# Kernel tuning notes

Hardware: AMD Instinct MI355X
Metric: run time of the kernel (lower is better)

The kernel has to match this reference:

```python
import jax, jax.numpy as jnp
import numpy as np

B, N, IN_C, HID_C, OUT_C = 64, 1024, 16, 64, 32


def process_graph(graph):
    # graph: [B, N, N]; add self-loops, then row-normalize by inverse degree.
    n = graph.shape[-1]
    g = graph + jnp.eye(n, dtype=graph.dtype)
    deg = jnp.sum(g, axis=-1)                      # [B, N]
    inv_deg = jnp.where(deg == 0, jnp.zeros_like(deg), 1.0 / deg)
    # diag(inv_deg) @ g == row-wise broadcast scale (avoids O(N^3) diag matmul)
    return g * inv_deg[..., None]                  # [B, N, N]


def setup_inputs() -> dict:
    key = jax.random.key(0)
    kx, kg, k1, kb1, k2, kb2 = jax.random.split(key, 6)
    x = jax.random.normal(kx, (B, N, IN_C), dtype=jnp.float32)
    graph = jax.random.uniform(kg, (B, N, N), dtype=jnp.float32)
    # nn.Linear default init: U(-1/sqrt(fan_in), 1/sqrt(fan_in))
    lim1 = 1.0 / np.sqrt(IN_C)
    W1 = jax.random.uniform(k1, (HID_C, IN_C), minval=-lim1, maxval=lim1, dtype=jnp.float32)
    b1 = jax.random.uniform(kb1, (HID_C,), minval=-lim1, maxval=lim1, dtype=jnp.float32)
    lim2 = 1.0 / np.sqrt(HID_C)
    W2 = jax.random.uniform(k2, (OUT_C, HID_C), minval=-lim2, maxval=lim2, dtype=jnp.float32)
    b2 = jax.random.uniform(kb2, (OUT_C,), minval=-lim2, maxval=lim2, dtype=jnp.float32)
    return {"x": x, "graph": graph, "W1": W1, "b1": b1, "W2": W2, "b2": b2}


def reference(x, graph, W1, b1, W2, b2):
    g = process_graph(graph)                                   # [B, N, N]
    h = jnp.einsum('bnc,hc->bnh', x, W1) + b1                  # linear_1
    h = jax.nn.relu(jnp.einsum('bnm,bmh->bnh', g, h))          # propagate + ReLU
    o = jnp.einsum('bnh,oh->bno', h, W2) + b2                  # linear_2
    o = jax.nn.relu(jnp.einsum('bnm,bmo->bno', g, o))          # propagate + ReLU
    return o                                                   # [B, N, OUT_C]
```

## Files before the change

### kernel.cpp

```cpp
#include <hip/hip_runtime.h>

typedef __attribute__((ext_vector_type(8))) short s16x8;
typedef __attribute__((ext_vector_type(8))) unsigned short u16x8;
typedef __attribute__((ext_vector_type(4))) float f32x4;

#define B_   64
#define N_   1024
#define CIN_ 16
#define CH_  64
#define CO_  32

__device__ __forceinline__ unsigned short f2bf(float f){
  unsigned int u = __float_as_uint(f);
  u += 0x7fffu + ((u >> 16) & 1u);
  return (unsigned short)(u >> 16);
}

__global__ __launch_bounds__(256) void k_linear1(
    const float* __restrict__ x, const float* __restrict__ W1,
    const float* __restrict__ b1, unsigned short* __restrict__ H1T){
  int gt   = blockIdx.x * 256 + threadIdx.x;
  int wave = gt >> 6;
  int lane = gt & 63;
  int b    = wave >> 4;
  int nl0  = (wave & 15) << 6;

  const float4* xv = (const float4*)(x + ((size_t)(b * N_ + nl0 + lane)) * CIN_);
  float xr[16];
#pragma unroll
  for (int i = 0; i < 4; ++i){
    float4 v = xv[i];
    xr[i*4+0] = v.x; xr[i*4+1] = v.y; xr[i*4+2] = v.z; xr[i*4+3] = v.w;
  }
  for (int h = 0; h < CH_; ++h){
    float acc = b1[h];
#pragma unroll
    for (int c = 0; c < CIN_; ++c) acc += xr[c] * W1[h * CIN_ + c];
    H1T[((size_t)(b * CH_ + h)) * N_ + nl0 + lane] = f2bf(acc);
  }
}

__global__ __launch_bounds__(256) void k_prop1(
    const float* __restrict__ graph, const unsigned short* __restrict__ H1T,
    const float* __restrict__ W2, const float* __restrict__ b2,
    unsigned short* __restrict__ O1T, float* __restrict__ idegw){
  __shared__ unsigned short sA[64 * 64];
  __shared__ unsigned short sB[64 * 64];
  __shared__ unsigned short sH2[64 * 64];
  __shared__ float sDegP[4 * 64];
  __shared__ float sIdeg[64];

  const int b    = blockIdx.x >> 4;
  const int mblk = blockIdx.x & 15;
  const int m0   = mblk << 6;
  const int tid  = threadIdx.x;
  const int lane = tid & 63, w = tid >> 6;
  const int l15  = lane & 15, lk = lane >> 4;
  const int srow = tid >> 2,  kq = tid & 3;
  const int gn   = m0 + srow;
  const int swzS = (srow & 7) << 3;
  const int swzF = (l15  & 7) << 3;

  const float*          gRow = graph + ((size_t)b << 20) + ((size_t)gn << 10) + (kq << 4);
  const unsigned short* hRow = H1T + ((size_t)(b * CH_ + srow)) * N_ + (kq << 4);

  float degp = 0.f;
  f32x4 acc[4] = {{0,0,0,0},{0,0,0,0},{0,0,0,0},{0,0,0,0}};

  float4 pg[4]; u16x8 ph[2];
  {
    const float4* gp = (const float4*)gRow;
#pragma unroll
    for (int i = 0; i < 4; ++i) pg[i] = gp[i];
    const u16x8* hp = (const u16x8*)hRow;
    ph[0] = hp[0]; ph[1] = hp[1];
  }

  for (int ks = 0; ks < 16; ++ks){
    float4 ng[4]; u16x8 nh[2];
    if (ks < 15){
      const float4* gp = (const float4*)(gRow + ((ks + 1) << 6));
#pragma unroll
      for (int i = 0; i < 4; ++i) ng[i] = gp[i];
      const u16x8* hp = (const u16x8*)(hRow + ((ks + 1) << 6));
      nh[0] = hp[0]; nh[1] = hp[1];
    } else {
#pragma unroll
      for (int i = 0; i < 4; ++i) ng[i] = pg[i];
      nh[0] = ph[0]; nh[1] = ph[1];
    }

    float vals[16];
#pragma unroll
    for (int i = 0; i < 4; ++i){
      float4 v = pg[i];
      if (ks == mblk){
        int gc = (ks << 6) + (kq << 4) + (i << 2);
        v.x += (gc + 0 == gn) ? 1.f : 0.f;
        v.y += (gc + 1 == gn) ? 1.f : 0.f;
        v.z += (gc + 2 == gn) ? 1.f : 0.f;
        v.w += (gc + 3 == gn) ? 1.f : 0.f;
      }
      degp += (v.x + v.y) + (v.z + v.w);
      vals[i*4+0] = v.x; vals[i*4+1] = v.y; vals[i*4+2] = v.z; vals[i*4+3] = v.w;
    }
    u16x8 pk0, pk1;
#pragma unroll
    for (int e = 0; e < 8; ++e){ pk0[e] = f2bf(vals[e]); pk1[e] = f2bf(vals[8 + e]); }
    *(u16x8*)&sA[srow * 64 + (((kq << 4) + 0) ^ swzS)] = pk0;
    *(u16x8*)&sA[srow * 64 + (((kq << 4) + 8) ^ swzS)] = pk1;
    *(u16x8*)&sB[srow * 64 + (((kq << 4) + 0) ^ swzS)] = ph[0];
    *(u16x8*)&sB[srow * 64 + (((kq << 4) + 8) ^ swzS)] = ph[1];
    __syncthreads();
#pragma unroll
    for (int kk = 0; kk < 2; ++kk){
      int ko = (kk << 5) + (lk << 3);
      s16x8 a = *(const s16x8*)&sA[((w << 4) + l15) * 64 + (ko ^ swzF)];
#pragma unroll
      for (int cf = 0; cf < 4; ++cf){
        s16x8 bb = *(const s16x8*)&sB[((cf << 4) + l15) * 64 + (ko ^ swzF)];
        acc[cf] = __builtin_amdgcn_mfma_f32_16x16x32_bf16(a, bb, acc[cf], 0, 0, 0);
      }
    }
    __syncthreads();
#pragma unroll
    for (int i = 0; i < 4; ++i) pg[i] = ng[i];
    ph[0] = nh[0]; ph[1] = nh[1];
  }

  sDegP[(kq << 6) + srow] = degp;
  __syncthreads();
  if (tid < 64){
    float d  = sDegP[tid] + sDegP[64 + tid] + sDegP[128 + tid] + sDegP[192 + tid];
    float id = 1.f / d;
    sIdeg[tid] = id;
    idegw[(b << 10) + m0 + tid] = id;
  }
  __syncthreads();

  f32x4 idv = *(const f32x4*)&sIdeg[(w << 4) + (lk << 2)];
#pragma unroll
  for (int cf = 0; cf < 4; ++cf){
#pragma unroll
    for (int j = 0; j < 4; ++j){
      float hv = acc[cf][j] * idv[j];
      hv = hv > 0.f ? hv : 0.f;
      int row = (w << 4) + (lk << 2) + j;
      int col = (cf << 4) + l15;
      sH2[row * 64 + (col ^ ((row & 7) << 3))] = f2bf(hv);
    }
  }
  __syncthreads();

  f32x4 acc2[2] = {{0,0,0,0},{0,0,0,0}};
#pragma unroll
  for (int kk = 0; kk < 2; ++kk){
    int ko = (kk << 5) + (lk << 3);
    s16x8 a2 = *(const s16x8*)&sH2[((w << 4) + l15) * 64 + (ko ^ swzF)];
#pragma unroll
    for (int cf = 0; cf < 2; ++cf){
      const float4* wv = (const float4*)(W2 + ((cf << 4) + l15) * CH_ + ko);
      float4 w0 = wv[0], w1 = wv[1];
      s16x8 bw;
      bw[0] = (short)f2bf(w0.x); bw[1] = (short)f2bf(w0.y);
      bw[2] = (short)f2bf(w0.z); bw[3] = (short)f2bf(w0.w);
      bw[4] = (short)f2bf(w1.x); bw[5] = (short)f2bf(w1.y);
      bw[6] = (short)f2bf(w1.z); bw[7] = (short)f2bf(w1.w);
      acc2[cf] = __builtin_amdgcn_mfma_f32_16x16x32_bf16(a2, bw, acc2[cf], 0, 0, 0);
    }
  }
#pragma unroll
  for (int cf = 0; cf < 2; ++cf){
    float badd = b2[(cf << 4) + l15];
#pragma unroll
    for (int j = 0; j < 4; ++j){
      float v = acc2[cf][j] + badd;
      int n = m0 + (w << 4) + (lk << 2) + j;
      O1T[((size_t)(b * CO_ + (cf << 4) + l15)) * N_ + n] = f2bf(v);
    }
  }
}

__global__ __launch_bounds__(256) void k_prop2(
    const float* __restrict__ graph, const unsigned short* __restrict__ O1T,
    const float* __restrict__ idegw, float* __restrict__ out){
  __shared__ unsigned short sA[64 * 64];
  __shared__ unsigned short sB[32 * 64];
  __shared__ float sIdeg[64];

  const int b    = blockIdx.x >> 4;
  const int mblk = blockIdx.x & 15;
  const int m0   = mblk << 6;
  const int tid  = threadIdx.x;
  const int lane = tid & 63, w = tid >> 6;
  const int l15  = lane & 15, lk = lane >> 4;
  const int srow = tid >> 2,  kq = tid & 3;
  const int gn   = m0 + srow;
  const int swzS = (srow & 7) << 3;
  const int swzF = (l15  & 7) << 3;

  if (tid < 64) sIdeg[tid] = idegw[(b << 10) + m0 + tid];

  const float* gRow = graph + ((size_t)b << 20) + ((size_t)gn << 10) + (kq << 4);
  const int bcolS = tid >> 3, bkq = tid & 7;
  const unsigned short* oRow = O1T + ((size_t)(b * CO_ + bcolS)) * N_ + (bkq << 3);
  const int swzB = (bcolS & 7) << 3;

  f32x4 acc[2] = {{0,0,0,0},{0,0,0,0}};

  float4 pg[4]; u16x8 po;
  {
    const float4* gp = (const float4*)gRow;
#pragma unroll
    for (int i = 0; i < 4; ++i) pg[i] = gp[i];
    po = *(const u16x8*)oRow;
  }

  for (int ks = 0; ks < 16; ++ks){
    float4 ng[4]; u16x8 no;
    if (ks < 15){
      const float4* gp = (const float4*)(gRow + ((ks + 1) << 6));
#pragma unroll
      for (int i = 0; i < 4; ++i) ng[i] = gp[i];
      no = *(const u16x8*)(oRow + ((ks + 1) << 6));
    } else {
#pragma unroll
      for (int i = 0; i < 4; ++i) ng[i] = pg[i];
      no = po;
    }

    float vals[16];
#pragma unroll
    for (int i = 0; i < 4; ++i){
      float4 v = pg[i];
      if (ks == mblk){
        int gc = (ks << 6) + (kq << 4) + (i << 2);
        v.x += (gc + 0 == gn) ? 1.f : 0.f;
        v.y += (gc + 1 == gn) ? 1.f : 0.f;
        v.z += (gc + 2 == gn) ? 1.f : 0.f;
        v.w += (gc + 3 == gn) ? 1.f : 0.f;
      }
      vals[i*4+0] = v.x; vals[i*4+1] = v.y; vals[i*4+2] = v.z; vals[i*4+3] = v.w;
    }
    u16x8 pk0, pk1;
#pragma unroll
    for (int e = 0; e < 8; ++e){ pk0[e] = f2bf(vals[e]); pk1[e] = f2bf(vals[8 + e]); }
    *(u16x8*)&sA[srow * 64 + (((kq << 4) + 0) ^ swzS)] = pk0;
    *(u16x8*)&sA[srow * 64 + (((kq << 4) + 8) ^ swzS)] = pk1;
    *(u16x8*)&sB[bcolS * 64 + ((bkq << 3) ^ swzB)] = po;
    __syncthreads();
#pragma unroll
    for (int kk = 0; kk < 2; ++kk){
      int ko = (kk << 5) + (lk << 3);
      s16x8 a = *(const s16x8*)&sA[((w << 4) + l15) * 64 + (ko ^ swzF)];
#pragma unroll
      for (int cf = 0; cf < 2; ++cf){
        s16x8 bb = *(const s16x8*)&sB[((cf << 4) + l15) * 64 + (ko ^ swzF)];
        acc[cf] = __builtin_amdgcn_mfma_f32_16x16x32_bf16(a, bb, acc[cf], 0, 0, 0);
      }
    }
    __syncthreads();
#pragma unroll
    for (int i = 0; i < 4; ++i) pg[i] = ng[i];
    po = no;
  }

  f32x4 idv = *(const f32x4*)&sIdeg[(w << 4) + (lk << 2)];
#pragma unroll
  for (int cf = 0; cf < 2; ++cf){
#pragma unroll
    for (int j = 0; j < 4; ++j){
      float v = acc[cf][j] * idv[j];
      v = v > 0.f ? v : 0.f;
      int n = m0 + (w << 4) + (lk << 2) + j;
      out[((size_t)(b * N_ + n)) * CO_ + (cf << 4) + l15] = v;
    }
  }
}

extern "C" void kernel_launch(void* const* d_in, const int* in_sizes, int n_in,
                              void* d_out, int out_size, void* d_ws, size_t ws_size,
                              hipStream_t stream){
  (void)in_sizes; (void)n_in; (void)out_size; (void)ws_size;
  const float* x     = (const float*)d_in[0];
  const float* graph = (const float*)d_in[1];
  const float* W1    = (const float*)d_in[2];
  const float* b1    = (const float*)d_in[3];
  const float* W2    = (const float*)d_in[4];
  const float* b2    = (const float*)d_in[5];
  float* out = (float*)d_out;

  unsigned short* H1T = (unsigned short*)d_ws;
  unsigned short* O1T = (unsigned short*)((char*)d_ws + ((size_t)8 << 20));
  float*        idegw = (float*)((char*)d_ws + ((size_t)12 << 20));

  k_linear1<<<256, 256, 0, stream>>>(x, W1, b1, H1T);
  k_prop1<<<B_ * 16, 256, 0, stream>>>(graph, H1T, W2, b2, O1T, idegw);
  k_prop2<<<B_ * 16, 256, 0, stream>>>(graph, O1T, idegw, out);
}
```

Measured before the change: 451.3 us.

## Load MFMA operands directly from global, dropping LDS staging and barriers

Both propagation kernels now have each lane load its MFMA A fragment (graph row slice) and B fragments (H1T/O1T) straight from global memory in register layout. This removes the LDS tile staging and the two block barriers per k-step. Degree is recomputed in each kernel with wave shuffles instead of being passed through workspace. Graph loads are nontemporal. Each lane's loads are now 32-byte strips per row rather than wide coalesced rows, the B operand is re-read by all four waves, and the loop runs twice as many shorter k-steps.

```diff
diff --git a/kernel.cpp b/kernel.cpp
--- a/kernel.cpp
+++ b/kernel.cpp
@@ -25,12 +25,13 @@
   int b    = wave >> 4;
   int nl0  = (wave & 15) << 6;
 
-  const float4* xv = (const float4*)(x + ((size_t)(b * N_ + nl0 + lane)) * CIN_);
+  const f32x4* xv = (const f32x4*)(x + ((size_t)(b * N_ + nl0 + lane)) * CIN_);
   float xr[16];
 #pragma unroll
   for (int i = 0; i < 4; ++i){
-    float4 v = xv[i];
-    xr[i*4+0] = v.x; xr[i*4+1] = v.y; xr[i*4+2] = v.z; xr[i*4+3] = v.w;
+    f32x4 v = xv[i];
+#pragma unroll
+    for (int e = 0; e < 4; ++e) xr[i*4+e] = v[e];
   }
   for (int h = 0; h < CH_; ++h){
     float acc = b1[h];
@@ -43,130 +44,94 @@
 __global__ __launch_bounds__(256) void k_prop1(
     const float* __restrict__ graph, const unsigned short* __restrict__ H1T,
     const float* __restrict__ W2, const float* __restrict__ b2,
-    unsigned short* __restrict__ O1T, float* __restrict__ idegw){
-  __shared__ unsigned short sA[64 * 64];
-  __shared__ unsigned short sB[64 * 64];
-  __shared__ unsigned short sH2[64 * 64];
-  __shared__ float sDegP[4 * 64];
-  __shared__ float sIdeg[64];
+    unsigned short* __restrict__ O1T){
+  __shared__ unsigned short sH2[4][16 * 64];
 
   const int b    = blockIdx.x >> 4;
-  const int mblk = blockIdx.x & 15;
-  const int m0   = mblk << 6;
+  const int m0   = (blockIdx.x & 15) << 6;
   const int tid  = threadIdx.x;
-  const int lane = tid & 63, w = tid >> 6;
+  const int w    = tid >> 6, lane = tid & 63;
   const int l15  = lane & 15, lk = lane >> 4;
-  const int srow = tid >> 2,  kq = tid & 3;
-  const int gn   = m0 + srow;
-  const int swzS = (srow & 7) << 3;
-  const int swzF = (l15  & 7) << 3;
-
-  const float*          gRow = graph + ((size_t)b << 20) + ((size_t)gn << 10) + (kq << 4);
-  const unsigned short* hRow = H1T + ((size_t)(b * CH_ + srow)) * N_ + (kq << 4);
-
-  float degp = 0.f;
+  const int gn   = m0 + (w << 4) + l15;
+  const int ksd  = (m0 + (w << 4)) >> 5;
+
+  const float* gA = graph + ((size_t)b << 20) + ((size_t)gn << 10) + (lk << 3);
+  const unsigned short* hB = H1T + (size_t)(b * CH_ + l15) * N_ + (lk << 3);
+
   f32x4 acc[4] = {{0,0,0,0},{0,0,0,0},{0,0,0,0},{0,0,0,0}};
-
-  float4 pg[4]; u16x8 ph[2];
-  {
-    const float4* gp = (const float4*)gRow;
-#pragma unroll
-    for (int i = 0; i < 4; ++i) pg[i] = gp[i];
-    const u16x8* hp = (const u16x8*)hRow;
-    ph[0] = hp[0]; ph[1] = hp[1];
-  }
-
-  for (int ks = 0; ks < 16; ++ks){
-    float4 ng[4]; u16x8 nh[2];
-    if (ks < 15){
-      const float4* gp = (const float4*)(gRow + ((ks + 1) << 6));
-#pragma unroll
-      for (int i = 0; i < 4; ++i) ng[i] = gp[i];
-      const u16x8* hp = (const u16x8*)(hRow + ((ks + 1) << 6));
-      nh[0] = hp[0]; nh[1] = hp[1];
-    } else {
-#pragma unroll
-      for (int i = 0; i < 4; ++i) ng[i] = pg[i];
-      nh[0] = ph[0]; nh[1] = ph[1];
-    }
-
-    float vals[16];
-#pragma unroll
-    for (int i = 0; i < 4; ++i){
-      float4 v = pg[i];
-      if (ks == mblk){
-        int gc = (ks << 6) + (kq << 4) + (i << 2);
-        v.x += (gc + 0 == gn) ? 1.f : 0.f;
-        v.y += (gc + 1 == gn) ? 1.f : 0.f;
-        v.z += (gc + 2 == gn) ? 1.f : 0.f;
-        v.w += (gc + 3 == gn) ? 1.f : 0.f;
-      }
-      degp += (v.x + v.y) + (v.z + v.w);
-      vals[i*4+0] = v.x; vals[i*4+1] = v.y; vals[i*4+2] = v.z; vals[i*4+3] = v.w;
-    }
-    u16x8 pk0, pk1;
-#pragma unroll
-    for (int e = 0; e < 8; ++e){ pk0[e] = f2bf(vals[e]); pk1[e] = f2bf(vals[8 + e]); }
-    *(u16x8*)&sA[srow * 64 + (((kq << 4) + 0) ^ swzS)] = pk0;
-    *(u16x8*)&sA[srow * 64 + (((kq << 4) + 8) ^ swzS)] = pk1;
-    *(u16x8*)&sB[srow * 64 + (((kq << 4) + 0) ^ swzS)] = ph[0];
-    *(u16x8*)&sB[srow * 64 + (((kq << 4) + 8) ^ swzS)] = ph[1];
-    __syncthreads();
-#pragma unroll
-    for (int kk = 0; kk < 2; ++kk){
-      int ko = (kk << 5) + (lk << 3);
-      s16x8 a = *(const s16x8*)&sA[((w << 4) + l15) * 64 + (ko ^ swzF)];
-#pragma unroll
-      for (int cf = 0; cf < 4; ++cf){
-        s16x8 bb = *(const s16x8*)&sB[((cf << 4) + l15) * 64 + (ko ^ swzF)];
-        acc[cf] = __builtin_amdgcn_mfma_f32_16x16x32_bf16(a, bb, acc[cf], 0, 0, 0);
-      }
-    }
-    __syncthreads();
-#pragma unroll
-    for (int i = 0; i < 4; ++i) pg[i] = ng[i];
-    ph[0] = nh[0]; ph[1] = nh[1];
-  }
-
-  sDegP[(kq << 6) + srow] = degp;
-  __syncthreads();
-  if (tid < 64){
-    float d  = sDegP[tid] + sDegP[64 + tid] + sDegP[128 + tid] + sDegP[192 + tid];
-    float id = 1.f / d;
-    sIdeg[tid] = id;
-    idegw[(b << 10) + m0 + tid] = id;
-  }
-  __syncthreads();
-
-  f32x4 idv = *(const f32x4*)&sIdeg[(w << 4) + (lk << 2)];
+  float deg = 0.f;
+
+  f32x4 a0 = __builtin_nontemporal_load((const f32x4*)(gA));
+  f32x4 a1 = __builtin_nontemporal_load((const f32x4*)(gA + 4));
+  u16x8 b0 = *(const u16x8*)(hB);
+  u16x8 b1f = *(const u16x8*)(hB + 16 * N_);
+  u16x8 b2f = *(const u16x8*)(hB + 32 * N_);
+  u16x8 b3f = *(const u16x8*)(hB + 48 * N_);
+
+  for (int ks = 0; ks < 32; ++ks){
+    const int kn = (((ks + 1) & 31) << 5);
+    f32x4 na0 = __builtin_nontemporal_load((const f32x4*)(gA + kn));
+    f32x4 na1 = __builtin_nontemporal_load((const f32x4*)(gA + kn + 4));
+    u16x8 nb0 = *(const u16x8*)(hB + kn);
+    u16x8 nb1 = *(const u16x8*)(hB + 16 * N_ + kn);
+    u16x8 nb2 = *(const u16x8*)(hB + 32 * N_ + kn);
+    u16x8 nb3 = *(const u16x8*)(hB + 48 * N_ + kn);
+
+    float va[8] = {a0[0], a0[1], a0[2], a0[3], a1[0], a1[1], a1[2], a1[3]};
+    if (ks == ksd){
+      const int d0 = (ks << 5) + (lk << 3);
+#pragma unroll
+      for (int e = 0; e < 8; ++e) va[e] += (d0 + e == gn) ? 1.f : 0.f;
+    }
+#pragma unroll
+    for (int e = 0; e < 8; ++e) deg += va[e];
+    s16x8 af;
+#pragma unroll
+    for (int e = 0; e < 8; ++e) af[e] = (short)f2bf(va[e]);
+
+    acc[0] = __builtin_amdgcn_mfma_f32_16x16x32_bf16(af, (s16x8)b0,  acc[0], 0, 0, 0);
+    acc[1] = __builtin_amdgcn_mfma_f32_16x16x32_bf16(af, (s16x8)b1f, acc[1], 0, 0, 0);
+    acc[2] = __builtin_amdgcn_mfma_f32_16x16x32_bf16(af, (s16x8)b2f, acc[2], 0, 0, 0);
+    acc[3] = __builtin_amdgcn_mfma_f32_16x16x32_bf16(af, (s16x8)b3f, acc[3], 0, 0, 0);
+
+    a0 = na0; a1 = na1; b0 = nb0; b1f = nb1; b2f = nb2; b3f = nb3;
+  }
+
+  deg += __shfl_xor(deg, 16);
+  deg += __shfl_xor(deg, 32);
+  float ideg = 1.f / deg;
+  float idv[4];
+#pragma unroll
+  for (int j = 0; j < 4; ++j) idv[j] = __shfl(ideg, (lk << 2) + j);
+
 #pragma unroll
   for (int cf = 0; cf < 4; ++cf){
 #pragma unroll
     for (int j = 0; j < 4; ++j){
       float hv = acc[cf][j] * idv[j];
       hv = hv > 0.f ? hv : 0.f;
-      int row = (w << 4) + (lk << 2) + j;
+      int row = (lk << 2) + j;
       int col = (cf << 4) + l15;
-      sH2[row * 64 + (col ^ ((row & 7) << 3))] = f2bf(hv);
+      sH2[w][(row << 6) + (col ^ ((row & 7) << 3))] = f2bf(hv);
     }
   }
   __syncthreads();
+  s16x8 a2[2];
+#pragma unroll
+  for (int kk = 0; kk < 2; ++kk)
+    a2[kk] = *(const s16x8*)&sH2[w][(l15 << 6) + (((kk << 5) + (lk << 3)) ^ ((l15 & 7) << 3))];
 
   f32x4 acc2[2] = {{0,0,0,0},{0,0,0,0}};
 #pragma unroll
   for (int kk = 0; kk < 2; ++kk){
-    int ko = (kk << 5) + (lk << 3);
-    s16x8 a2 = *(const s16x8*)&sH2[((w << 4) + l15) * 64 + (ko ^ swzF)];
 #pragma unroll
     for (int cf = 0; cf < 2; ++cf){
-      const float4* wv = (const float4*)(W2 + ((cf << 4) + l15) * CH_ + ko);
-      float4 w0 = wv[0], w1 = wv[1];
+      const f32x4* wp = (const f32x4*)(W2 + ((cf << 4) + l15) * CH_ + (kk << 5) + (lk << 3));
+      f32x4 w0 = wp[0], w1 = wp[1];
       s16x8 bw;
-      bw[0] = (short)f2bf(w0.x); bw[1] = (short)f2bf(w0.y);
-      bw[2] = (short)f2bf(w0.z); bw[3] = (short)f2bf(w0.w);
-      bw[4] = (short)f2bf(w1.x); bw[5] = (short)f2bf(w1.y);
-      bw[6] = (short)f2bf(w1.z); bw[7] = (short)f2bf(w1.w);
-      acc2[cf] = __builtin_amdgcn_mfma_f32_16x16x32_bf16(a2, bw, acc2[cf], 0, 0, 0);
+#pragma unroll
+      for (int e = 0; e < 4; ++e){ bw[e] = (short)f2bf(w0[e]); bw[4 + e] = (short)f2bf(w1[e]); }
+      acc2[cf] = __builtin_amdgcn_mfma_f32_16x16x32_bf16(a2[kk], bw, acc2[cf], 0, 0, 0);
     }
   }
 #pragma unroll
@@ -183,89 +148,58 @@
 
 __global__ __launch_bounds__(256) void k_prop2(
     const float* __restrict__ graph, const unsigned short* __restrict__ O1T,
-    const float* __restrict__ idegw, float* __restrict__ out){
-  __shared__ unsigned short sA[64 * 64];
-  __shared__ unsigned short sB[32 * 64];
-  __shared__ float sIdeg[64];
-
+    float* __restrict__ out){
   const int b    = blockIdx.x >> 4;
-  const int mblk = blockIdx.x & 15;
-  const int m0   = mblk << 6;
+  const int m0   = (blockIdx.x & 15) << 6;
   const int tid  = threadIdx.x;
-  const int lane = tid & 63, w = tid >> 6;
+  const int w    = tid >> 6, lane = tid & 63;
   const int l15  = lane & 15, lk = lane >> 4;
-  const int srow = tid >> 2,  kq = tid & 3;
-  const int gn   = m0 + srow;
-  const int swzS = (srow & 7) << 3;
-  const int swzF = (l15  & 7) << 3;
-
-  if (tid < 64) sIdeg[tid] = idegw[(b << 10) + m0 + tid];
-
-  const float* gRow = graph + ((size_t)b << 20) + ((size_t)gn << 10) + (kq << 4);
-  const int bcolS = tid >> 3, bkq = tid & 7;
-  const unsigned short* oRow = O1T + ((size_t)(b * CO_ + bcolS)) * N_ + (bkq << 3);
-  const int swzB = (bcolS & 7) << 3;
+  const int gn   = m0 + (w << 4) + l15;
+  const int ksd  = (m0 + (w << 4)) >> 5;
+
+  const float* gA = graph + ((size_t)b << 20) + ((size_t)gn << 10) + (lk << 3);
+  const unsigned short* oB = O1T + (size_t)(b * CO_ + l15) * N_ + (lk << 3);
 
   f32x4 acc[2] = {{0,0,0,0},{0,0,0,0}};
-
-  float4 pg[4]; u16x8 po;
-  {
-    const float4* gp = (const float4*)gRow;
-#pragma unroll
-    for (int i = 0; i < 4; ++i) pg[i] = gp[i];
-    po = *(const u16x8*)oRow;
-  }
-
-  for (int ks = 0; ks < 16; ++ks){
-    float4 ng[4]; u16x8 no;
-    if (ks < 15){
-      const float4* gp = (const float4*)(gRow + ((ks + 1) << 6));
-#pragma unroll
-      for (int i = 0; i < 4; ++i) ng[i] = gp[i];
-      no = *(const u16x8*)(oRow + ((ks + 1) << 6));
-    } else {
-#pragma unroll
-      for (int i = 0; i < 4; ++i) ng[i] = pg[i];
-      no = po;
-    }
-
-    float vals[16];
-#pragma unroll
-    for (int i = 0; i < 4; ++i){
-      float4 v = pg[i];
-      if (ks == mblk){
-        int gc = (ks << 6) + (kq << 4) + (i << 2);
-        v.x += (gc + 0 == gn) ? 1.f : 0.f;
-        v.y += (gc + 1 == gn) ? 1.f : 0.f;
-        v.z += (gc + 2 == gn) ? 1.f : 0.f;
-        v.w += (gc + 3 == gn) ? 1.f : 0.f;
-      }
-      vals[i*4+0] = v.x; vals[i*4+1] = v.y; vals[i*4+2] = v.z; vals[i*4+3] = v.w;
-    }
-    u16x8 pk0, pk1;
-#pragma unroll
-    for (int e = 0; e < 8; ++e){ pk0[e] = f2bf(vals[e]); pk1[e] = f2bf(vals[8 + e]); }
-    *(u16x8*)&sA[srow * 64 + (((kq << 4) + 0) ^ swzS)] = pk0;
-    *(u16x8*)&sA[srow * 64 + (((kq << 4) + 8) ^ swzS)] = pk1;
-    *(u16x8*)&sB[bcolS * 64 + ((bkq << 3) ^ swzB)] = po;
-    __syncthreads();
-#pragma unroll
-    for (int kk = 0; kk < 2; ++kk){
-      int ko = (kk << 5) + (lk << 3);
-      s16x8 a = *(const s16x8*)&sA[((w << 4) + l15) * 64 + (ko ^ swzF)];
-#pragma unroll
-      for (int cf = 0; cf < 2; ++cf){
-        s16x8 bb = *(const s16x8*)&sB[((cf << 4) + l15) * 64 + (ko ^ swzF)];
-        acc[cf] = __builtin_amdgcn_mfma_f32_16x16x32_bf16(a, bb, acc[cf], 0, 0, 0);
-      }
-    }
-    __syncthreads();
-#pragma unroll
-    for (int i = 0; i < 4; ++i) pg[i] = ng[i];
-    po = no;
-  }
-
-  f32x4 idv = *(const f32x4*)&sIdeg[(w << 4) + (lk << 2)];
+  float deg = 0.f;
+
+  f32x4 a0 = __builtin_nontemporal_load((const f32x4*)(gA));
+  f32x4 a1 = __builtin_nontemporal_load((const f32x4*)(gA + 4));
+  u16x8 b0 = *(const u16x8*)(oB);
+  u16x8 b1f = *(const u16x8*)(oB + 16 * N_);
+
+  for (int ks = 0; ks < 32; ++ks){
+    const int kn = (((ks + 1) & 31) << 5);
+    f32x4 na0 = __builtin_nontemporal_load((const f32x4*)(gA + kn));
+    f32x4 na1 = __builtin_nontemporal_load((const f32x4*)(gA + kn + 4));
+    u16x8 nb0 = *(const u16x8*)(oB + kn);
+    u16x8 nb1 = *(const u16x8*)(oB + 16 * N_ + kn);
+
+    float va[8] = {a0[0], a0[1], a0[2], a0[3], a1[0], a1[1], a1[2], a1[3]};
+    if (ks == ksd){
+      const int d0 = (ks << 5) + (lk << 3);
+#pragma unroll
+      for (int e = 0; e < 8; ++e) va[e] += (d0 + e == gn) ? 1.f : 0.f;
+    }
+#pragma unroll
+    for (int e = 0; e < 8; ++e) deg += va[e];
+    s16x8 af;
+#pragma unroll
+    for (int e = 0; e < 8; ++e) af[e] = (short)f2bf(va[e]);
+
+    acc[0] = __builtin_amdgcn_mfma_f32_16x16x32_bf16(af, (s16x8)b0,  acc[0], 0, 0, 0);
+    acc[1] = __builtin_amdgcn_mfma_f32_16x16x32_bf16(af, (s16x8)b1f, acc[1], 0, 0, 0);
+
+    a0 = na0; a1 = na1; b0 = nb0; b1f = nb1;
+  }
+
+  deg += __shfl_xor(deg, 16);
+  deg += __shfl_xor(deg, 32);
+  float ideg = 1.f / deg;
+  float idv[4];
+#pragma unroll
+  for (int j = 0; j < 4; ++j) idv[j] = __shfl(ideg, (lk << 2) + j);
+
 #pragma unroll
   for (int cf = 0; cf < 2; ++cf){
 #pragma unroll
@@ -292,9 +226,8 @@
 
   unsigned short* H1T = (unsigned short*)d_ws;
   unsigned short* O1T = (unsigned short*)((char*)d_ws + ((size_t)8 << 20));
-  float*        idegw = (float*)((char*)d_ws + ((size_t)12 << 20));
 
   k_linear1<<<256, 256, 0, stream>>>(x, W1, b1, H1T);
-  k_prop1<<<B_ * 16, 256, 0, stream>>>(graph, H1T, W2, b2, O1T, idegw);
-  k_prop2<<<B_ * 16, 256, 0, stream>>>(graph, O1T, idegw, out);
-}
+  k_prop1<<<B_ * 16, 256, 0, stream>>>(graph, H1T, W2, b2, O1T);
+  k_prop2<<<B_ * 16, 256, 0, stream>>>(graph, O1T, out);
+}
```

Measured after the change: 526.5 us. 16.6% more time.
